# Kernel tuning notes

Hardware: AMD Instinct MI355X
Metric: run time of the kernel (lower is better)

Reference implementation:

```python
import jax, jax.numpy as jnp
import numpy as np
import math

EMBED_DIM = 768
NUM_HEADS = 12
HEAD_DIM = EMBED_DIM // NUM_HEADS
EPS = 1e-6


def setup_inputs() -> dict:
    key = jax.random.key(0)
    ks = jax.random.split(key, 9)
    T, B, N, D = 4, 4, 1024, EMBED_DIM
    s = 0.02
    return {
        "x": jax.random.normal(ks[0], (T, B, N, D), dtype=jnp.float32),
        "Wq": jax.random.normal(ks[1], (D, D), dtype=jnp.float32) * s,
        "bq": jax.random.normal(ks[2], (D,), dtype=jnp.float32) * s,
        "Wk": jax.random.normal(ks[3], (D, D), dtype=jnp.float32) * s,
        "bk": jax.random.normal(ks[4], (D,), dtype=jnp.float32) * s,
        "Wv": jax.random.normal(ks[5], (D, D), dtype=jnp.float32) * s,
        "bv": jax.random.normal(ks[6], (D,), dtype=jnp.float32) * s,
        "Wo": jax.random.normal(ks[7], (D, D), dtype=jnp.float32) * s,
        "bo": jax.random.normal(ks[8], (D,), dtype=jnp.float32) * s,
    }


def _split_heads(y, T, B, N):
    # [T,B,N,D] -> [T,B,H,N,Dh]
    return y.reshape(T, B, N, NUM_HEADS, HEAD_DIM).transpose(0, 1, 3, 2, 4)


def reference(x, Wq, bq, Wk, bk, Wv, bv, Wo, bo):
    T, B, N, D = x.shape
    # q/k/v projections (nn.Linear: x @ W^T + b)
    q = _split_heads(x @ Wq.T + bq, T, B, N)
    k = _split_heads(x @ Wk.T + bk, T, B, N)
    v = _split_heads(x @ Wv.T + bv, T, B, N)
    # scores = q k^T / sqrt(head_dim)
    scores = jnp.einsum("tbhnd,tbhmd->tbhnm", q, k) / math.sqrt(HEAD_DIM)
    # spike-form normalization: relu then L1-normalize along keys
    act = jax.nn.relu(scores)
    attn = act / (act.sum(axis=-1, keepdims=True) + EPS)
    ctx = jnp.einsum("tbhnm,tbhmd->tbhnd", attn, v)
    # merge heads: [T,B,H,N,Dh] -> [T,B,N,D]
    out = ctx.transpose(0, 1, 3, 2, 4).reshape(T, B, N, D)
    return out @ Wo.T + bo
```

## Files before the change

kernel.cpp:

```cpp
#include <hip/hip_runtime.h>
#include <hip/hip_bf16.h>
#include <cstdint>


typedef __attribute__((ext_vector_type(8))) short short8;
typedef __attribute__((ext_vector_type(4))) float float4v;
typedef __attribute__((ext_vector_type(16))) float float16v;

__device__ __forceinline__ unsigned short f2bf(float f) {
  unsigned int u = __float_as_uint(f);
  u = (u + 0x7fffu + ((u >> 16) & 1u)) >> 16;
  return (unsigned short)u;
}

__device__ __forceinline__ unsigned int pkbf(float a, float b) {
  unsigned int ua = __float_as_uint(a) + 0x8000u;
  unsigned int ub = __float_as_uint(b) + 0x8000u;
  return __builtin_amdgcn_perm(ub, ua, 0x07060302u);
}

__device__ __forceinline__ void gld_lds16(const void* g, void* lds) {
  __builtin_amdgcn_global_load_lds(
      (__attribute__((address_space(1))) void*)(uintptr_t)g,
      (__attribute__((address_space(3))) void*)(uint32_t)(uintptr_t)lds,
      16, 0, 0);
}

__global__ __launch_bounds__(256) void cast4(const float* __restrict__ src,
                                             unsigned short* __restrict__ dst,
                                             int n4) {
  int i = blockIdx.x * 256 + threadIdx.x;
  if (i >= n4) return;
  float4 f = reinterpret_cast<const float4*>(src)[i];
  ushort4 o;
  o.x = f2bf(f.x); o.y = f2bf(f.y); o.z = f2bf(f.z); o.w = f2bf(f.w);
  reinterpret_cast<ushort4*>(dst)[i] = o;
}

template <bool OUT_BF16>
__global__ __launch_bounds__(256) void gemm_bt(
    const unsigned short* __restrict__ A,
    const unsigned short* __restrict__ Bt,
    unsigned short* __restrict__ Cb,
    float* __restrict__ Cf,
    const float* __restrict__ b0, const float* __restrict__ b1,
    const float* __restrict__ b2, int N) {
  constexpr int K = 768;
  __shared__ unsigned short As[128 * 32];
  __shared__ unsigned short Bs[128 * 32];

  const int tid = threadIdx.x;
  const int lane = tid & 63;
  const int w = tid >> 6;
  const int wrow = w >> 1, wcol = w & 1;
  const int l15 = lane & 15, quad = lane >> 4;
  const int i0 = blockIdx.y * 128, j0 = blockIdx.x * 128;

  const unsigned short* ga = A + (size_t)(i0 + 32 * w + (lane >> 2)) * K + (lane & 3) * 8;
  const unsigned short* gb = Bt + (size_t)(j0 + 32 * w + (lane >> 2)) * K + (lane & 3) * 8;

  float4v acc[4][4];
#pragma unroll
  for (int a = 0; a < 4; ++a)
#pragma unroll
    for (int b = 0; b < 4; ++b) acc[a][b] = float4v{0.f, 0.f, 0.f, 0.f};

#pragma unroll 1
  for (int kt = 0; kt < K / 32; ++kt) {
    const unsigned short* pa = ga + kt * 32;
    const unsigned short* pb = gb + kt * 32;
    gld_lds16(pa, &As[(32 * w) * 32]);
    gld_lds16(pa + 16 * K, &As[(32 * w + 16) * 32]);
    gld_lds16(pb, &Bs[(32 * w) * 32]);
    gld_lds16(pb + 16 * K, &Bs[(32 * w + 16) * 32]);
    __syncthreads();

    short8 af[4], bfr[4];
#pragma unroll
    for (int a = 0; a < 4; ++a)
      af[a] = *(const short8*)&As[(wrow * 64 + a * 16 + l15) * 32 + quad * 8];
#pragma unroll
    for (int b = 0; b < 4; ++b)
      bfr[b] = *(const short8*)&Bs[(wcol * 64 + b * 16 + l15) * 32 + quad * 8];
#pragma unroll
    for (int a = 0; a < 4; ++a)
#pragma unroll
      for (int b = 0; b < 4; ++b)
        acc[a][b] = __builtin_amdgcn_mfma_f32_16x16x32_bf16(af[a], bfr[b], acc[a][b], 0, 0, 0);
    __syncthreads();
  }

  const int sel = j0 / 768;
  const float* bp = (sel == 0) ? b0 : ((sel == 1) ? b1 : b2);
#pragma unroll
  for (int a = 0; a < 4; ++a) {
    const int row0 = i0 + wrow * 64 + a * 16 + quad * 4;
#pragma unroll
    for (int b = 0; b < 4; ++b) {
      const int col = j0 + wcol * 64 + b * 16 + l15;
      const float bias = bp[col - sel * 768];
#pragma unroll
      for (int r = 0; r < 4; ++r) {
        const float v = acc[a][b][r] + bias;
        if (OUT_BF16)
          Cb[(size_t)(row0 + r) * N + col] = f2bf(v);
        else
          Cf[(size_t)(row0 + r) * N + col] = v;
      }
    }
  }
}

__global__ __launch_bounds__(256) void transpose_v(
    const unsigned short* __restrict__ qkv, unsigned short* __restrict__ vt) {
  __shared__ unsigned short T[64 * 72];
  const int bz = blockIdx.x;
  const int nt = bz & 15;
  const int tbh = bz >> 4;
  const int tb = tbh / 12, h = tbh % 12;
  const int tid = threadIdx.x;
#pragma unroll
  for (int it = 0; it < 2; ++it) {
    int c = tid + it * 256;
    int row = c >> 3, d0 = (c & 7) * 8;
    const unsigned short* g =
        qkv + (size_t)(tb * 1024 + nt * 64 + row) * 2304 + 1536 + h * 64 + d0;
    *(uint4*)&T[row * 72 + d0] = *(const uint4*)g;
  }
  __syncthreads();
#pragma unroll
  for (int it = 0; it < 2; ++it) {
    int c = tid + it * 256;
    int d = c >> 3, n0 = (c & 7) * 8;
    unsigned short tmp[8];
#pragma unroll
    for (int i = 0; i < 8; ++i) tmp[i] = T[(n0 + i) * 72 + d];
    *(uint4*)&vt[((size_t)(tb * 12 + h) * 64 + d) * 1024 + nt * 64 + n0] =
        *(uint4*)tmp;
  }
}

__global__ __launch_bounds__(256) void attn32(
    const unsigned short* __restrict__ qkv,
    const unsigned short* __restrict__ vt,
    unsigned short* __restrict__ ctx) {
  __shared__ unsigned short QP[128 * 72];
  __shared__ unsigned short Ks[64 * 72];
  __shared__ unsigned short Vs[64 * 72];

  const int qt = blockIdx.x;
  const int tbh = blockIdx.y;
  const int tb = tbh / 12, h = tbh % 12;
  const int tid = threadIdx.x, lane = tid & 63, w = tid >> 6;
  const int l31 = lane & 31, hl = lane >> 5;

#pragma unroll
  for (int it = 0; it < 4; ++it) {
    int c = it * 256 + tid;
    int row = c >> 3, col = (c & 7) * 8;
    *(uint4*)&QP[row * 72 + col] = *(const uint4*)(
        qkv + (size_t)(tb * 1024 + qt * 128 + row) * 2304 + h * 64 + col);
  }
  __syncthreads();

  short8 qf[4];
#pragma unroll
  for (int kc = 0; kc < 4; ++kc)
    qf[kc] = *(const short8*)&QP[(w * 32 + l31) * 72 + kc * 16 + hl * 8];
  unsigned short* PW = &QP[(w * 32) * 72];

  float16v octx[2];
#pragma unroll
  for (int i = 0; i < 16; ++i) { octx[0][i] = 0.f; octx[1][i] = 0.f; }
  float den = 0.f;

#pragma unroll 1
  for (int kv = 0; kv < 16; ++kv) {
    __syncthreads();
#pragma unroll
    for (int it = 0; it < 2; ++it) {
      int c = it * 256 + tid;
      int row = c >> 3, col = (c & 7) * 8;
      *(uint4*)&Ks[row * 72 + col] = *(const uint4*)(
          qkv + (size_t)(tb * 1024 + kv * 64 + row) * 2304 + 768 + h * 64 + col);
      *(uint4*)&Vs[row * 72 + col] = *(const uint4*)(
          vt + ((size_t)(tb * 12 + h) * 64 + row) * 1024 + kv * 64 + col);
    }
    __syncthreads();

#pragma unroll
    for (int mt = 0; mt < 2; ++mt) {
      float16v st;
#pragma unroll
      for (int i = 0; i < 16; ++i) st[i] = 0.f;
#pragma unroll
      for (int kc = 0; kc < 4; ++kc) {
        short8 af = *(const short8*)&Ks[(mt * 32 + l31) * 72 + kc * 16 + hl * 8];
        st = __builtin_amdgcn_mfma_f32_32x32x16_bf16(af, qf[kc], st, 0, 0, 0);
      }
#pragma unroll
      for (int g = 0; g < 4; ++g) {
        float v0 = st[4 * g + 0]; v0 = v0 > 0.f ? v0 : 0.f;
        float v1 = st[4 * g + 1]; v1 = v1 > 0.f ? v1 : 0.f;
        float v2 = st[4 * g + 2]; v2 = v2 > 0.f ? v2 : 0.f;
        float v3 = st[4 * g + 3]; v3 = v3 > 0.f ? v3 : 0.f;
        den += (v0 + v1) + (v2 + v3);
        uint2 u;
        u.x = pkbf(v0, v1);
        u.y = pkbf(v2, v3);
        *(uint2*)&PW[l31 * 72 + mt * 32 + g * 8 + hl * 4] = u;
      }
    }

    short8 pa[4];
#pragma unroll
    for (int kc = 0; kc < 4; ++kc)
      pa[kc] = *(const short8*)&PW[l31 * 72 + kc * 16 + hl * 8];
#pragma unroll
    for (int dt = 0; dt < 2; ++dt)
#pragma unroll
      for (int kc = 0; kc < 4; ++kc) {
        short8 vb = *(const short8*)&Vs[(dt * 32 + l31) * 72 + kc * 16 + hl * 8];
        octx[dt] = __builtin_amdgcn_mfma_f32_32x32x16_bf16(pa[kc], vb, octx[dt], 0, 0, 0);
      }
  }

  den += __shfl_xor(den, 32);
  __syncthreads();
  float* dsc = (float*)Ks;
  if (hl == 0) dsc[w * 32 + l31] = 1.f / (den + 8e-6f);
  __syncthreads();

#pragma unroll
  for (int dt = 0; dt < 2; ++dt)
#pragma unroll
    for (int reg = 0; reg < 16; ++reg) {
      const int qrow = (reg & 3) + 8 * (reg >> 2) + 4 * hl;
      const float sc = dsc[w * 32 + qrow];
      const int grow = tb * 1024 + qt * 128 + w * 32 + qrow;
      ctx[(size_t)grow * 768 + h * 64 + dt * 32 + l31] =
          f2bf(octx[dt][reg] * sc);
    }
}

extern "C" void kernel_launch(void* const* d_in, const int* in_sizes, int n_in,
                              void* d_out, int out_size, void* d_ws, size_t ws_size,
                              hipStream_t stream) {
  const float* x  = (const float*)d_in[0];
  const float* Wq = (const float*)d_in[1];
  const float* bq = (const float*)d_in[2];
  const float* Wk = (const float*)d_in[3];
  const float* bk = (const float*)d_in[4];
  const float* Wv = (const float*)d_in[5];
  const float* bv = (const float*)d_in[6];
  const float* Wo = (const float*)d_in[7];
  const float* bo = (const float*)d_in[8];
  float* out = (float*)d_out;

  char* ws = (char*)d_ws;
  unsigned short* XBF  = (unsigned short*)(ws);
  unsigned short* CTX  = (unsigned short*)(ws);
  unsigned short* WQKV = (unsigned short*)(ws + 25165824);
  unsigned short* WOb  = (unsigned short*)(ws + 28704768);
  unsigned short* QKV  = (unsigned short*)(ws + 29884416);
  unsigned short* VT   = (unsigned short*)(ws + 105381888);

  cast4<<<12288, 256, 0, stream>>>(x, XBF, 3145728);
  cast4<<<576, 256, 0, stream>>>(Wq, WQKV, 147456);
  cast4<<<576, 256, 0, stream>>>(Wk, WQKV + 589824, 147456);
  cast4<<<576, 256, 0, stream>>>(Wv, WQKV + 1179648, 147456);
  cast4<<<576, 256, 0, stream>>>(Wo, WOb, 147456);

  gemm_bt<true><<<dim3(18, 128), 256, 0, stream>>>(XBF, WQKV, QKV, nullptr,
                                                   bq, bk, bv, 2304);
  transpose_v<<<3072, 256, 0, stream>>>(QKV, VT);
  attn32<<<dim3(8, 192), 256, 0, stream>>>(QKV, VT, CTX);
  gemm_bt<false><<<dim3(6, 128), 256, 0, stream>>>(CTX, WOb, nullptr, out,
                                                   bo, bo, bo, 768);
}
```

Measured before the change: 342.9 us.

## Double-buffer K/V via direct-to-LDS loads and widen attention query tiles

```diff
diff --git a/kernel.cpp b/kernel.cpp
--- a/kernel.cpp
+++ b/kernel.cpp
@@ -140,13 +140,13 @@
   }
 }
 
-__global__ __launch_bounds__(256) void attn32(
+__global__ __launch_bounds__(256, 3) void attn32(
     const unsigned short* __restrict__ qkv,
     const unsigned short* __restrict__ vt,
     unsigned short* __restrict__ ctx) {
-  __shared__ unsigned short QP[128 * 72];
-  __shared__ unsigned short Ks[64 * 72];
-  __shared__ unsigned short Vs[64 * 72];
+  __shared__ unsigned short Ks[2][64 * 64];
+  __shared__ unsigned short Vs[2][64 * 64];
+  __shared__ unsigned short Pb[4 * 32 * 72];
 
   const int qt = blockIdx.x;
   const int tbh = blockIdx.y;
@@ -154,93 +154,119 @@
   const int tid = threadIdx.x, lane = tid & 63, w = tid >> 6;
   const int l31 = lane & 31, hl = lane >> 5;
 
-#pragma unroll
-  for (int it = 0; it < 4; ++it) {
-    int c = it * 256 + tid;
-    int row = c >> 3, col = (c & 7) * 8;
-    *(uint4*)&QP[row * 72 + col] = *(const uint4*)(
-        qkv + (size_t)(tb * 1024 + qt * 128 + row) * 2304 + h * 64 + col);
-  }
-  __syncthreads();
-
-  short8 qf[4];
-#pragma unroll
-  for (int kc = 0; kc < 4; ++kc)
-    qf[kc] = *(const short8*)&QP[(w * 32 + l31) * 72 + kc * 16 + hl * 8];
-  unsigned short* PW = &QP[(w * 32) * 72];
-
-  float16v octx[2];
-#pragma unroll
-  for (int i = 0; i < 16; ++i) { octx[0][i] = 0.f; octx[1][i] = 0.f; }
-  float den = 0.f;
+  short8 qf[2][4];
+#pragma unroll
+  for (int qs = 0; qs < 2; ++qs) {
+    const size_t qrow = (size_t)(tb * 1024 + qt * 256 + w * 64 + qs * 32 + l31);
+#pragma unroll
+    for (int kc = 0; kc < 4; ++kc)
+      qf[qs][kc] =
+          *(const short8*)(qkv + qrow * 2304 + h * 64 + kc * 16 + hl * 8);
+  }
+
+  const int sr = (lane >> 3);
+  const int sblk = lane & 7;
+  unsigned short* PW = &Pb[w * 32 * 72];
+
+  float16v octx[2][2];
+#pragma unroll
+  for (int qs = 0; qs < 2; ++qs)
+#pragma unroll
+    for (int dt = 0; dt < 2; ++dt)
+#pragma unroll
+      for (int i = 0; i < 16; ++i) octx[qs][dt][i] = 0.f;
+  float den[2] = {0.f, 0.f};
+
+  auto stage = [&](int kv, int buf) {
+#pragma unroll
+    for (int t = 0; t < 2; ++t) {
+      const int r = w * 16 + t * 8 + sr;
+      const int c = sblk ^ (r & 7);
+      gld_lds16(qkv + (size_t)(tb * 1024 + kv * 64 + r) * 2304 + 768 + h * 64 + c * 8,
+                &Ks[buf][(w * 16 + t * 8) * 64]);
+      gld_lds16(vt + ((size_t)tbh * 64 + r) * 1024 + kv * 64 + c * 8,
+                &Vs[buf][(w * 16 + t * 8) * 64]);
+    }
+  };
+
+  stage(0, 0);
 
 #pragma unroll 1
   for (int kv = 0; kv < 16; ++kv) {
+    const int cur = kv & 1;
     __syncthreads();
-#pragma unroll
-    for (int it = 0; it < 2; ++it) {
-      int c = it * 256 + tid;
-      int row = c >> 3, col = (c & 7) * 8;
-      *(uint4*)&Ks[row * 72 + col] = *(const uint4*)(
-          qkv + (size_t)(tb * 1024 + kv * 64 + row) * 2304 + 768 + h * 64 + col);
-      *(uint4*)&Vs[row * 72 + col] = *(const uint4*)(
-          vt + ((size_t)(tb * 12 + h) * 64 + row) * 1024 + kv * 64 + col);
+    if (kv < 15) stage(kv + 1, cur ^ 1);
+
+    short8 vf[2][4];
+#pragma unroll
+    for (int dt = 0; dt < 2; ++dt) {
+      const int r = dt * 32 + l31;
+#pragma unroll
+      for (int kc = 0; kc < 4; ++kc)
+        vf[dt][kc] =
+            *(const short8*)&Vs[cur][r * 64 + (((kc * 2 + hl) ^ (r & 7)) * 8)];
     }
-    __syncthreads();
-
-#pragma unroll
-    for (int mt = 0; mt < 2; ++mt) {
-      float16v st;
-#pragma unroll
-      for (int i = 0; i < 16; ++i) st[i] = 0.f;
-#pragma unroll
-      for (int kc = 0; kc < 4; ++kc) {
-        short8 af = *(const short8*)&Ks[(mt * 32 + l31) * 72 + kc * 16 + hl * 8];
-        st = __builtin_amdgcn_mfma_f32_32x32x16_bf16(af, qf[kc], st, 0, 0, 0);
+
+#pragma unroll
+    for (int qs = 0; qs < 2; ++qs) {
+#pragma unroll
+      for (int mt = 0; mt < 2; ++mt) {
+        float16v st;
+#pragma unroll
+        for (int i = 0; i < 16; ++i) st[i] = 0.f;
+        const int r = mt * 32 + l31;
+#pragma unroll
+        for (int kc = 0; kc < 4; ++kc) {
+          short8 kf =
+              *(const short8*)&Ks[cur][r * 64 + (((kc * 2 + hl) ^ (r & 7)) * 8)];
+          st = __builtin_amdgcn_mfma_f32_32x32x16_bf16(kf, qf[qs][kc], st, 0, 0, 0);
+        }
+#pragma unroll
+        for (int g = 0; g < 4; ++g) {
+          float v0 = st[4 * g + 0]; v0 = v0 > 0.f ? v0 : 0.f;
+          float v1 = st[4 * g + 1]; v1 = v1 > 0.f ? v1 : 0.f;
+          float v2 = st[4 * g + 2]; v2 = v2 > 0.f ? v2 : 0.f;
+          float v3 = st[4 * g + 3]; v3 = v3 > 0.f ? v3 : 0.f;
+          den[qs] += (v0 + v1) + (v2 + v3);
+          uint2 u;
+          u.x = pkbf(v0, v1);
+          u.y = pkbf(v2, v3);
+          *(uint2*)&PW[l31 * 72 + mt * 32 + g * 8 + hl * 4] = u;
+        }
       }
-#pragma unroll
-      for (int g = 0; g < 4; ++g) {
-        float v0 = st[4 * g + 0]; v0 = v0 > 0.f ? v0 : 0.f;
-        float v1 = st[4 * g + 1]; v1 = v1 > 0.f ? v1 : 0.f;
-        float v2 = st[4 * g + 2]; v2 = v2 > 0.f ? v2 : 0.f;
-        float v3 = st[4 * g + 3]; v3 = v3 > 0.f ? v3 : 0.f;
-        den += (v0 + v1) + (v2 + v3);
-        uint2 u;
-        u.x = pkbf(v0, v1);
-        u.y = pkbf(v2, v3);
-        *(uint2*)&PW[l31 * 72 + mt * 32 + g * 8 + hl * 4] = u;
+      short8 pa[4];
+#pragma unroll
+      for (int kc = 0; kc < 4; ++kc)
+        pa[kc] = *(const short8*)&PW[l31 * 72 + kc * 16 + hl * 8];
+#pragma unroll
+      for (int dt = 0; dt < 2; ++dt)
+#pragma unroll
+        for (int kc = 0; kc < 4; ++kc)
+          octx[qs][dt] = __builtin_amdgcn_mfma_f32_32x32x16_bf16(
+              pa[kc], vf[dt][kc], octx[qs][dt], 0, 0, 0);
+    }
+  }
+
+#pragma unroll
+  for (int qs = 0; qs < 2; ++qs) den[qs] += __shfl_xor(den[qs], 32);
+  float* dsc = (float*)&Ks[0][0];
+  if (hl == 0) {
+    dsc[w * 64 + l31]      = 1.f / (den[0] + 8e-6f);
+    dsc[w * 64 + 32 + l31] = 1.f / (den[1] + 8e-6f);
+  }
+
+#pragma unroll
+  for (int qs = 0; qs < 2; ++qs)
+#pragma unroll
+    for (int dt = 0; dt < 2; ++dt)
+#pragma unroll
+      for (int reg = 0; reg < 16; ++reg) {
+        const int qrow = (reg & 3) + 8 * (reg >> 2) + 4 * hl;
+        const float sc = dsc[w * 64 + qs * 32 + qrow];
+        const size_t grow =
+            (size_t)(tb * 1024 + qt * 256 + w * 64 + qs * 32 + qrow);
+        ctx[grow * 768 + h * 64 + dt * 32 + l31] = f2bf(octx[qs][dt][reg] * sc);
       }
-    }
-
-    short8 pa[4];
-#pragma unroll
-    for (int kc = 0; kc < 4; ++kc)
-      pa[kc] = *(const short8*)&PW[l31 * 72 + kc * 16 + hl * 8];
-#pragma unroll
-    for (int dt = 0; dt < 2; ++dt)
-#pragma unroll
-      for (int kc = 0; kc < 4; ++kc) {
-        short8 vb = *(const short8*)&Vs[(dt * 32 + l31) * 72 + kc * 16 + hl * 8];
-        octx[dt] = __builtin_amdgcn_mfma_f32_32x32x16_bf16(pa[kc], vb, octx[dt], 0, 0, 0);
-      }
-  }
-
-  den += __shfl_xor(den, 32);
-  __syncthreads();
-  float* dsc = (float*)Ks;
-  if (hl == 0) dsc[w * 32 + l31] = 1.f / (den + 8e-6f);
-  __syncthreads();
-
-#pragma unroll
-  for (int dt = 0; dt < 2; ++dt)
-#pragma unroll
-    for (int reg = 0; reg < 16; ++reg) {
-      const int qrow = (reg & 3) + 8 * (reg >> 2) + 4 * hl;
-      const float sc = dsc[w * 32 + qrow];
-      const int grow = tb * 1024 + qt * 128 + w * 32 + qrow;
-      ctx[(size_t)grow * 768 + h * 64 + dt * 32 + l31] =
-          f2bf(octx[dt][reg] * sc);
-    }
 }
 
 extern "C" void kernel_launch(void* const* d_in, const int* in_sizes, int n_in,
@@ -274,7 +300,7 @@
   gemm_bt<true><<<dim3(18, 128), 256, 0, stream>>>(XBF, WQKV, QKV, nullptr,
                                                    bq, bk, bv, 2304);
   transpose_v<<<3072, 256, 0, stream>>>(QKV, VT);
-  attn32<<<dim3(8, 192), 256, 0, stream>>>(QKV, VT, CTX);
+  attn32<<<dim3(4, 192), 256, 0, stream>>>(QKV, VT, CTX);
   gemm_bt<false><<<dim3(6, 128), 256, 0, stream>>>(CTX, WOb, nullptr, out,
                                                    bo, bo, bo, 768);
 }
```

Measured after the change: 395.2 us. 1.15x slower.
